# Kernel tuning notes

Measured on AMD Instinct MI355X. Metric: run time of the kernel, lower is better.

## Reference

```python
import jax, jax.numpy as jnp
import numpy as np

B, C, Hh, Ww = 32, 512, 6, 40
NC = 97   # num classes; padding_idx = NC-1, start_idx = NC-2
L = 26    # label length (max_len+1); decoder tokens T = L+1 = 27


def _lstm2(x, layers):
    """2-layer unidirectional LSTM, batch_first, PyTorch gate order (i,f,g,o).
    x: (B,T,D); layers: list of (Wih, Whh, bih, bhh). Returns (B,T,H)."""
    h = x
    for (Wih, Whh, bih, bhh) in layers:
        Hd = Whh.shape[1]
        b = bih + bhh
        def step(carry, xt, Wih=Wih, Whh=Whh, b=b):
            hh, cc = carry
            g = xt @ Wih.T + hh @ Whh.T + b
            i, f, gg, o = jnp.split(g, 4, axis=-1)
            cc = jax.nn.sigmoid(f) * cc + jax.nn.sigmoid(i) * jnp.tanh(gg)
            hh = jax.nn.sigmoid(o) * jnp.tanh(cc)
            return (hh, cc), hh
        init = (jnp.zeros((h.shape[0], Hd), h.dtype), jnp.zeros((h.shape[0], Hd), h.dtype))
        _, ys = jax.lax.scan(step, init, jnp.swapaxes(h, 0, 1))
        h = jnp.swapaxes(ys, 0, 1)
    return h


def setup_inputs() -> dict:
    key = jax.random.key(0)
    it = iter(jax.random.split(key, 48))
    def nrm(shape, s=0.02):
        return jax.random.normal(next(it), shape, jnp.float32) * s
    d = {}
    d['feat'] = jax.random.normal(next(it), (B, C, Hh, Ww), jnp.float32)
    d['label'] = jax.random.randint(next(it), (B, L), 0, NC)
    d['valid_ratios'] = jax.random.uniform(next(it), (B,), jnp.float32, 0.5, 1.0)
    # encoder LSTM (2 layers, 512->512)
    for p in ['e0', 'e1']:
        d[p + '_Wih'] = nrm((4 * C, C)); d[p + '_Whh'] = nrm((4 * C, C))
        d[p + '_bih'] = jnp.zeros((4 * C,), jnp.float32); d[p + '_bhh'] = jnp.zeros((4 * C,), jnp.float32)
    d['enc_W'] = nrm((C, C)); d['enc_b'] = jnp.zeros((C,), jnp.float32)
    # attention: query 1x1 (Linear), key conv3x3, score 1x1 (Linear d->1)
    d['q_W'] = nrm((C, C)); d['q_b'] = jnp.zeros((C,), jnp.float32)
    d['k_W'] = nrm((C, C, 3, 3)); d['k_b'] = jnp.zeros((C,), jnp.float32)
    d['s_W'] = nrm((1, C)); d['s_b'] = jnp.zeros((1,), jnp.float32)
    emb = nrm((NC, C), 1.0)
    d['emb'] = emb.at[NC - 1].set(0.0)  # padding_idx row is zero
    # decoder LSTM (2 layers, 512->512)
    for p in ['d0', 'd1']:
        d[p + '_Wih'] = nrm((4 * C, C)); d[p + '_Whh'] = nrm((4 * C, C))
        d[p + '_bih'] = jnp.zeros((4 * C,), jnp.float32); d[p + '_bhh'] = jnp.zeros((4 * C,), jnp.float32)
    d['pred_W'] = nrm((NC, 3 * C)); d['pred_b'] = jnp.zeros((NC,), jnp.float32)
    return d


def reference(feat, label, valid_ratios,
              e0_Wih, e0_Whh, e0_bih, e0_bhh, e1_Wih, e1_Whh, e1_bih, e1_bhh,
              enc_W, enc_b, q_W, q_b, k_W, k_b, s_W, s_b, emb,
              d0_Wih, d0_Whh, d0_bih, d0_bhh, d1_Wih, d1_Whh, d1_bih, d1_bhh,
              pred_W, pred_b):
    # --- SAREncoder: max-pool over height, 2-layer LSTM, linear on last step ---
    feat_v = jnp.max(feat, axis=2).transpose(0, 2, 1)  # (B, W, C)
    hf = _lstm2(feat_v, [(e0_Wih, e0_Whh, e0_bih, e0_bhh), (e1_Wih, e1_Whh, e1_bih, e1_bhh)])
    holistic = hf[:, -1, :] @ enc_W.T + enc_b  # (B, C)
    # --- tokens: [holistic, embed(label)] ---
    tok = jnp.concatenate([holistic[:, None, :], emb[label]], axis=1)  # (B, T=L+1, C)
    Hid = _lstm2(tok, [(d0_Wih, d0_Whh, d0_bih, d0_bhh), (d1_Wih, d1_Whh, d1_bih, d1_bhh)])
    # --- 2D additive attention ---
    q = Hid @ q_W.T + q_b  # (B, T, C)
    k = jax.lax.conv_general_dilated(feat, k_W, (1, 1), 'SAME',
                                     dimension_numbers=('NCHW', 'OIHW', 'NCHW')) + k_b[None, :, None, None]
    t = jnp.tanh(k[:, None] + q[:, :, :, None, None])  # (B, T, C, h, w) big intermediate
    score = jnp.einsum('btchw,c->bthw', t, s_W[0]) + s_b[0]  # (B, T, h, w)
    vw = jnp.minimum(Ww, jnp.ceil(Ww * valid_ratios)).astype(jnp.int32)  # (B,)
    colmask = jnp.arange(Ww)[None, :] >= vw[:, None]  # (B, w)
    score = jnp.where(colmask[:, None, None, :], -jnp.inf, score)
    T = score.shape[1]
    aw = jax.nn.softmax(score.reshape(score.shape[0], T, -1), axis=-1).reshape(score.shape[0], T, Hh, Ww)
    attn_feat = jnp.einsum('bchw,bthw->btc', feat, aw)  # (B, T, C)
    # --- prediction (pred_concat=True); dropout is identity (deterministic) ---
    hol = jnp.broadcast_to(holistic[:, None, :], Hid.shape)
    preds = jnp.concatenate([Hid, attn_feat, hol], axis=-1) @ pred_W.T + pred_b
    return preds[:, 1:, :]  # (B, L, NC)
```

## Files before the change

### kernel.cpp

```cpp
#include <hip/hip_runtime.h>

typedef unsigned short u16;
typedef __attribute__((ext_vector_type(8))) short short8;
typedef __attribute__((ext_vector_type(4))) float floatx4;
typedef _Float16 half8 __attribute__((ext_vector_type(8)));
typedef _Float16 half2v __attribute__((ext_vector_type(2)));
typedef unsigned uint4v __attribute__((ext_vector_type(4)));

#define AGENT __HIP_MEMORY_SCOPE_AGENT
#define SENT 0x7FFF7FFFu

__device__ __forceinline__ float bf2f(u16 v) { return __uint_as_float(((unsigned)v) << 16); }
__device__ __forceinline__ u16 f2bf(float f) {
    unsigned u = __float_as_uint(f);
    unsigned r = (u + 0x7FFFu + ((u >> 16) & 1u)) >> 16;
    return (u16)r;
}
__device__ __forceinline__ float sigm_(float x) {
    return __builtin_amdgcn_rcpf(1.f + __expf(-x));
}
__device__ __forceinline__ float tanh_(float x) {
    x = fminf(fmaxf(x, -15.f), 15.f);
    float e = __expf(2.f * x);
    return (e - 1.f) * __builtin_amdgcn_rcpf(e + 1.f);
}

typedef __attribute__((address_space(1))) void gvoid_t;
typedef __attribute__((address_space(3))) void lvoid_t;
__device__ __forceinline__ void gl_lds16(const void* g, void* l) {
    __builtin_amdgcn_global_load_lds((gvoid_t*)g, (lvoid_t*)l, 16, 0, 0);
}

#define HEX_WORDS (134 * 32 * 256)

struct SrcPtrs {
    const void* e0Wih; const void* e1Wih; const void* d0Wih; const void* d1Wih;
    const void* b0; const void* b1; const void* b2; const void* b3;
    const void* b4; const void* b5; const void* b6; const void* b7;
    const void* encW; const void* qW; const void* predW; const void* emb;
    const void* encb; const void* qb; const void* kb; const void* sW;
    const void* sb; const void* predb;
};
#define OFF_W0      0
#define OFF_W1      1048576
#define OFF_W2      2097152
#define OFF_W3      3145728
#define OFF_B       4194304
#define OFF_ENCW    4210688
#define OFF_QW      4472832
#define OFF_PREDW   4734976
#define OFF_EMB     4883968
#define OFF_ENCB    4933632
#define OFF_QB      4934144
#define OFF_KB      4934656
#define OFF_SW      4935168
#define OFF_SB      4935680
#define OFF_PREDB   4935681
#define CANON_TOTAL 4935778

__device__ __forceinline__ int sniff_(const void* feat_raw) {
    const u16* p = (const u16*)feat_raw;
    int insane = 0;
    #pragma unroll
    for (int i = 0; i < 32; i += 2) {
        float x = bf2f(p[i]);
        float a = fabsf(x);
        if (!(a <= 1000.f)) insane = 1;
        if (x != 0.f && a < 1e-8f) insane = 1;
    }
    return insane;
}

struct PrepArgs {
    SrcPtrs S;
    const void* feat_raw;
    const void* vr_src;
    const void* kW_src;
    const void* wq_s0; const void* wq_s1; const void* wq_s2; const void* wq_s3;
    int* flag;
    unsigned* hEx;
    u16* canon;
    float* cvr;
    u16* W2;
    _Float16* wq_d0; _Float16* wq_d1; _Float16* wq_d2; _Float16* wq_d3;
    u16* featv;
    u16* featP;
};

#define PB_INIT    0
#define PB_CANON   4288
#define PB_CANONF  23569
#define PB_W2      23570
#define PB_WQ3     32786
#define PB_FEATP   34834
#define PB_TOTAL   35346

__global__ __launch_bounds__(256) void prep_all(PrepArgs P)
{
    const int blk = blockIdx.x;
    const int tid = threadIdx.x;

    if (blk < PB_CANON) {
        int idx = blk * 256 + tid;
        P.hEx[idx] = SENT;
        if (idx == 0) *P.flag = sniff_(P.feat_raw);
        return;
    }
    const int fl = sniff_(P.feat_raw);

    if (blk < PB_CANONF) {
        int idx = (blk - PB_CANON) * 256 + tid;
        if (idx >= CANON_TOTAL) return;
        const SrcPtrs& S = P.S;
        const void* s; int loc;
        if (idx < OFF_B) {
            int k = idx >> 20; loc = idx & 1048575;
            s = (k == 0) ? S.e0Wih : (k == 1) ? S.e1Wih : (k == 2) ? S.d0Wih : S.d1Wih;
        } else if (idx < OFF_ENCW) {
            int r = idx - OFF_B; int k = r >> 11; loc = r & 2047;
            s = (k == 0) ? S.b0 : (k == 1) ? S.b1 : (k == 2) ? S.b2 : (k == 3) ? S.b3
              : (k == 4) ? S.b4 : (k == 5) ? S.b5 : (k == 6) ? S.b6 : S.b7;
        } else if (idx < OFF_QW)    { s = S.encW;  loc = idx - OFF_ENCW; }
        else if (idx < OFF_PREDW)   { s = S.qW;    loc = idx - OFF_QW; }
        else if (idx < OFF_EMB)     { s = S.predW; loc = idx - OFF_PREDW; }
        else if (idx < OFF_ENCB)    { s = S.emb;   loc = idx - OFF_EMB; }
        else if (idx < OFF_QB)      { s = S.encb;  loc = idx - OFF_ENCB; }
        else if (idx < OFF_KB)      { s = S.qb;    loc = idx - OFF_QB; }
        else if (idx < OFF_SW)      { s = S.kb;    loc = idx - OFF_KB; }
        else if (idx < OFF_SB)      { s = S.sW;    loc = idx - OFF_SW; }
        else if (idx < OFF_PREDB)   { s = S.sb;    loc = idx - OFF_SB; }
        else                        { s = S.predb; loc = idx - OFF_PREDB; }
        P.canon[idx] = fl ? f2bf(((const float*)s)[loc]) : ((const u16*)s)[loc];
    } else if (blk == PB_CANONF) {
        if (tid < 32)
            P.cvr[tid] = fl ? ((const float*)P.vr_src)[tid] : bf2f(((const u16*)P.vr_src)[tid]);
    } else if (blk < PB_WQ3) {
        int idx = (blk - PB_W2) * 256 + tid;
        int co = idx / 4608;
        int r = idx % 4608;
        int kh = r / 1536;
        int r2 = r % 1536;
        int kw = r2 / 512;
        int ci = r2 & 511;
        long si = ((long)(co * 512 + ci) * 3 + kh) * 3 + kw;
        P.W2[idx] = fl ? f2bf(((const float*)P.kW_src)[si]) : ((const u16*)P.kW_src)[si];
    } else if (blk < PB_FEATP) {
        int gb = blk - PB_WQ3;
        int id = gb >> 9;
        const void* W = (id == 0) ? P.wq_s0 : (id == 1) ? P.wq_s1 : (id == 2) ? P.wq_s2 : P.wq_s3;
        _Float16* D = (id == 0) ? P.wq_d0 : (id == 1) ? P.wq_d1 : (id == 2) ? P.wq_d2 : P.wq_d3;
        int o = (gb & 511) * 256 + tid;
        int t = o & 511;
        int c = (o >> 9) & 31;
        int j = o >> 14;
        int rid = t >> 1, hf = t & 1;
        int n = (rid >> 6) * 512 + j * 64 + (rid & 63);
        int k = hf * 256 + c * 8;
        _Float16* dst = D + (long)o * 8;
        #pragma unroll
        for (int jj = 0; jj < 8; jj++) {
            long si = (long)n * 512 + k + jj;
            float v = fl ? ((const float*)W)[si] : bf2f(((const u16*)W)[si]);
            dst[jj] = (_Float16)v;
        }
    } else {
        __shared__ u16 S[32][242];
        int q = blk - PB_FEATP;
        int b = q >> 4;
        int c0 = (q & 15) * 32;
        long gbase = ((long)b * 512 + c0) * 240;
        for (int i = tid; i < 32 * 240; i += 256) {
            float x = fl ? ((const float*)P.feat_raw)[gbase + i] : bf2f(((const u16*)P.feat_raw)[gbase + i]);
            S[i / 240][i % 240] = f2bf(x);
        }
        __syncthreads();
        for (int i = tid; i < 40 * 32; i += 256) {
            int w = i >> 5, c = i & 31;
            float mx = bf2f(S[c][w]);
            #pragma unroll
            for (int h = 1; h < 6; h++) mx = fmaxf(mx, bf2f(S[c][h * 40 + w]));
            P.featv[((long)(b * 40 + w)) * 512 + c0 + c] = f2bf(mx);
        }
        for (int i = tid; i < 6 * 40 * 32; i += 256) {
            int c = i & 31; int r = i >> 5;
            int wp1 = r % 40, hp1 = r / 40;
            P.featP[((long)(b * 8 + hp1 + 1) * 42 + (wp1 + 1)) * 512 + c0 + c] = S[c][hp1 * 40 + wp1];
        }
        for (int i = tid; i < 96 * 32; i += 256) {
            int c = i & 31; int r = i >> 5;
            int hp, wp;
            if (r < 42)      { hp = 0; wp = r; }
            else if (r < 84) { hp = 7; wp = r - 42; }
            else             { int q2 = r - 84; hp = 1 + (q2 >> 1); wp = (q2 & 1) * 41; }
            P.featP[((long)(b * 8 + hp) * 42 + wp) * 512 + c0 + c] = 0;
        }
    }
}

__global__ __launch_bounds__(256) void gemm_nt_f32(
    const u16* __restrict__ A, int lda,
    const u16* __restrict__ Bw,
    const u16* __restrict__ bias0, const u16* __restrict__ bias1,
    float* __restrict__ C, int M, int N, int K, int ldc)
{
    __shared__ __align__(16) u16 As[64][40];
    __shared__ __align__(16) u16 Bs[64][40];
    const int tid = threadIdx.x;
    const int bn = blockIdx.x, bm = blockIdx.y;
    const int l = tid & 63, wid = tid >> 6;
    const int wm = wid >> 1, wn = wid & 1;
    const int lr = tid >> 2, lc = (tid & 3) * 8;
    const int l15 = l & 15, lq = l >> 4;

    floatx4 acc00 = (floatx4)(0.f), acc01 = (floatx4)(0.f), acc10 = (floatx4)(0.f), acc11 = (floatx4)(0.f);

    int am = bm * 64 + lr; if (am > M - 1) am = M - 1;
    const u16* Ap = A + (long)am * lda + lc;
    const u16* Bp = Bw + (long)(bn * 64 + lr) * K + lc;

    for (int k0 = 0; k0 < K; k0 += 32) {
        *(short8*)&As[lr][lc] = *(const short8*)(Ap + k0);
        *(short8*)&Bs[lr][lc] = *(const short8*)(Bp + k0);
        __syncthreads();
        short8 af0 = *(const short8*)&As[wm * 32 + l15][lq * 8];
        short8 af1 = *(const short8*)&As[wm * 32 + 16 + l15][lq * 8];
        short8 bf0 = *(const short8*)&Bs[wn * 32 + l15][lq * 8];
        short8 bf1 = *(const short8*)&Bs[wn * 32 + 16 + l15][lq * 8];
        acc00 = __builtin_amdgcn_mfma_f32_16x16x32_bf16(af0, bf0, acc00, 0, 0, 0);
        acc01 = __builtin_amdgcn_mfma_f32_16x16x32_bf16(af0, bf1, acc01, 0, 0, 0);
        acc10 = __builtin_amdgcn_mfma_f32_16x16x32_bf16(af1, bf0, acc10, 0, 0, 0);
        acc11 = __builtin_amdgcn_mfma_f32_16x16x32_bf16(af1, bf1, acc11, 0, 0, 0);
        __syncthreads();
    }
    floatx4 accs[2][2] = {{acc00, acc01}, {acc10, acc11}};
    #pragma unroll
    for (int i = 0; i < 2; i++)
        #pragma unroll
        for (int j = 0; j < 2; j++)
            #pragma unroll
            for (int r = 0; r < 4; r++) {
                int gm = bm * 64 + wm * 32 + i * 16 + lq * 4 + r;
                int gn = bn * 64 + wn * 32 + j * 16 + l15;
                if (gm < M) {
                    float v = accs[i][j][r];
                    if (bias0) v += bf2f(bias0[gn]);
                    if (bias1) v += bf2f(bias1[gn]);
                    C[(long)gm * ldc + gn] = v;
                }
            }
}

__device__ __forceinline__ void gemm128_body(
    u16* lds, const u16* __restrict__ A, const u16* __restrict__ Bw,
    const u16* __restrict__ bias0, const u16* __restrict__ bias1,
    float* __restrict__ C, int M, int ldc, int bn, int bm)
{
    u16 (*As)[128][32] = (u16(*)[128][32])lds;
    u16 (*Bs)[128][32] = (u16(*)[128][32])(lds + 4 * 128 * 32);
    const int tid = threadIdx.x;
    const int wv = tid >> 6, l = tid & 63;
    const int wm = wv >> 2, wn = wv & 3;
    const int l15 = l & 15, lq = l >> 4;
    const int ch = ((l & 3) ^ ((l >> 3) & 3)) * 8;

    int ar = bm * 128 + wv * 16 + (l >> 2);
    if (ar > M - 1) ar = M - 1;
    const u16* ga = A + (long)ar * 512 + ch;
    const u16* gb = Bw + (long)(bn * 128 + wv * 16 + (l >> 2)) * 512 + ch;

    floatx4 acc[4][2];
    #pragma unroll
    for (int i = 0; i < 4; i++)
        #pragma unroll
        for (int j = 0; j < 2; j++) acc[i][j] = (floatx4)(0.f);

    auto stage = [&](int k0, int pb) {
        gl_lds16(ga + k0, &As[pb][wv * 16][0]);
        gl_lds16(gb + k0, &Bs[pb][wv * 16][0]);
    };
    const int rs = (lq ^ ((l15 >> 1) & 3)) * 8;
    auto compute = [&](int cur) {
        short8 af[4], bf[2];
        #pragma unroll
        for (int i = 0; i < 4; i++) af[i] = *(const short8*)&As[cur][wm * 64 + i * 16 + l15][rs];
        #pragma unroll
        for (int j = 0; j < 2; j++) bf[j] = *(const short8*)&Bs[cur][wn * 32 + j * 16 + l15][rs];
        #pragma unroll
        for (int i = 0; i < 4; i++)
            #pragma unroll
            for (int j = 0; j < 2; j++)
                acc[i][j] = __builtin_amdgcn_mfma_f32_16x16x32_bf16(af[i], bf[j], acc[i][j], 0, 0, 0);
    };

    stage(0, 0); stage(32, 1); stage(64, 2);
    for (int k = 0; k < 14; k++) {
        asm volatile("s_waitcnt vmcnt(4)" ::: "memory");
        __builtin_amdgcn_s_barrier();
        asm volatile("" ::: "memory");
        if (k < 13) stage((k + 3) * 32, (k + 3) & 3);
        compute(k & 3);
    }
    asm volatile("s_waitcnt vmcnt(2)" ::: "memory");
    __builtin_amdgcn_s_barrier();
    asm volatile("" ::: "memory");
    compute(2);
    asm volatile("s_waitcnt vmcnt(0)" ::: "memory");
    __builtin_amdgcn_s_barrier();
    asm volatile("" ::: "memory");
    compute(3);

    #pragma unroll
    for (int i = 0; i < 4; i++)
        #pragma unroll
        for (int j = 0; j < 2; j++)
            #pragma unroll
            for (int r = 0; r < 4; r++) {
                int gm = bm * 128 + wm * 64 + i * 16 + lq * 4 + r;
                int gn = bn * 128 + wn * 32 + j * 16 + l15;
                if (gm < M) {
                    float v = acc[i][j][r];
                    if (bias0) v += bf2f(bias0[gn]);
                    if (bias1) v += bf2f(bias1[gn]);
                    C[(long)gm * ldc + gn] = v;
                }
            }
}

__device__ __forceinline__ void conv_body(
    u16* lds, const u16* __restrict__ featP, const u16* __restrict__ W2,
    const u16* __restrict__ kb, u16* __restrict__ kmap, int bx, int by)
{
    u16 (*As)[128][32] = (u16(*)[128][32])lds;
    u16 (*Bs)[128][32] = (u16(*)[128][32])(lds + 4 * 128 * 32);
    const int tid = threadIdx.x;
    int bm = bx * 8 + (by & 7);
    int bn = by >> 3;
    if (bm >= 60) return;
    const int wv = tid >> 6, l = tid & 63;
    const int wm = wv >> 2, wn = wv & 3;
    const int l15 = l & 15, lq = l >> 4;
    const int ch = ((l & 3) ^ ((l >> 3) & 3)) * 8;

    int ar = bm * 128 + wv * 16 + (l >> 2);
    int ab = ar / 240, ahw = ar % 240;
    const u16* ga = featP + ((long)(ab * 8 + ahw / 40) * 42 + (ahw % 40)) * 512 + ch;
    const u16* gb = W2 + (long)(bn * 128 + wv * 16 + (l >> 2)) * 4608 + ch;

    floatx4 acc[4][2];
    #pragma unroll
    for (int i = 0; i < 4; i++)
        #pragma unroll
        for (int j = 0; j < 2; j++) acc[i][j] = (floatx4)(0.f);

    auto stage = [&](int k0, int pb) {
        int kh = k0 / 1536;
        int rem = k0 - kh * 1536;
        int aoff = (kh * 42 + (rem >> 9)) * 512 + (rem & 511);
        gl_lds16(ga + aoff, &As[pb][wv * 16][0]);
        gl_lds16(gb + k0, &Bs[pb][wv * 16][0]);
    };
    const int rs = (lq ^ ((l15 >> 1) & 3)) * 8;
    auto compute = [&](int cur) {
        short8 af[4], bf[2];
        #pragma unroll
        for (int i = 0; i < 4; i++) af[i] = *(const short8*)&As[cur][wm * 64 + i * 16 + l15][rs];
        #pragma unroll
        for (int j = 0; j < 2; j++) bf[j] = *(const short8*)&Bs[cur][wn * 32 + j * 16 + l15][rs];
        #pragma unroll
        for (int i = 0; i < 4; i++)
            #pragma unroll
            for (int j = 0; j < 2; j++)
                acc[i][j] = __builtin_amdgcn_mfma_f32_16x16x32_bf16(af[i], bf[j], acc[i][j], 0, 0, 0);
    };

    stage(0, 0); stage(32, 1); stage(64, 2);
    for (int k = 0; k < 142; k++) {
        asm volatile("s_waitcnt vmcnt(4)" ::: "memory");
        __builtin_amdgcn_s_barrier();
        asm volatile("" ::: "memory");
        if (k < 141) stage((k + 3) * 32, (k + 3) & 3);
        compute(k & 3);
    }
    asm volatile("s_waitcnt vmcnt(2)" ::: "memory");
    __builtin_amdgcn_s_barrier();
    asm volatile("" ::: "memory");
    compute(2);
    asm volatile("s_waitcnt vmcnt(0)" ::: "memory");
    __builtin_amdgcn_s_barrier();
    asm volatile("" ::: "memory");
    compute(3);

    #pragma unroll
    for (int i = 0; i < 4; i++)
        #pragma unroll
        for (int j = 0; j < 2; j++)
            #pragma unroll
            for (int r = 0; r < 4; r++) {
                int row = bm * 128 + wm * 64 + i * 16 + lq * 4 + r;
                int col = bn * 128 + wn * 32 + j * 16 + l15;
                kmap[(long)row * 512 + col] = f2bf(acc[i][j][r] + bf2f(kb[col]));
            }
}

__global__ __launch_bounds__(512) void gemm_nt_128(
    const u16* __restrict__ A, const u16* __restrict__ Bw,
    const u16* __restrict__ bias0, const u16* __restrict__ bias1,
    float* __restrict__ C, int M, int ldc)
{
    extern __shared__ u16 ldsb[];
    gemm128_body(ldsb, A, Bw, bias0, bias1, C, M, ldc, blockIdx.x, blockIdx.y);
}

__global__ __launch_bounds__(512) void qf_conv(
    const u16* __restrict__ Hid, const u16* __restrict__ qW,
    const u16* __restrict__ qb, float* __restrict__ qf,
    const u16* __restrict__ featP, const u16* __restrict__ W2,
    const u16* __restrict__ kb, u16* __restrict__ kmap)
{
    extern __shared__ u16 ldsb[];
    int q = blockIdx.x;
    if (q < 28) {
        gemm128_body(ldsb, Hid, qW, qb, nullptr, qf, 864, 512, q & 3, q >> 2);
    } else {
        int c = q - 28;
        conv_body(ldsb, featP, W2, kb, kmap, c & 7, c >> 3);
    }
}

#define WL(F) F(0) F(1) F(2) F(3) F(4) F(5) F(6) F(7) F(8) F(9) F(10) F(11) F(12) F(13) F(14) F(15) \
              F(16) F(17) F(18) F(19) F(20) F(21) F(22) F(23) F(24) F(25) F(26) F(27) F(28) F(29) F(30) F(31)
#define WLA(F) F(0,0) F(1,1) F(2,2) F(3,3) F(4,0) F(5,1) F(6,2) F(7,3) \
               F(8,0) F(9,1) F(10,2) F(11,3) F(12,0) F(13,1) F(14,2) F(15,3) \
               F(16,0) F(17,1) F(18,2) F(19,3) F(20,0) F(21,1) F(22,2) F(23,3) \
               F(24,0) F(25,1) F(26,2) F(27,3) F(28,0) F(29,1) F(30,2) F(31,3)
#define WDECL(i) half8 w##i = wp8[(long)(j * 32 + i) * 512 + tid];
#define WPIN(i)  asm volatile("" : "+v"(w##i));
#define DOTC(i,k) { \
    half8 hv = *(const half8*)&hS2[(hf * 2 + (i / 16)) * 136 + (i % 16) * 8]; \
    a##k = __builtin_amdgcn_fdot2(__builtin_shufflevector(hv, hv, 0, 1), __builtin_shufflevector(w##i, w##i, 0, 1), a##k, false); \
    a##k = __builtin_amdgcn_fdot2(__builtin_shufflevector(hv, hv, 2, 3), __builtin_shufflevector(w##i, w##i, 2, 3), a##k, false); \
    a##k = __builtin_amdgcn_fdot2(__builtin_shufflevector(hv, hv, 4, 5), __builtin_shufflevector(w##i, w##i, 4, 5), a##k, false); \
    a##k = __builtin_amdgcn_fdot2(__builtin_shufflevector(hv, hv, 6, 7), __builtin_shufflevector(w##i, w##i, 6, 7), a##k, false); }

__global__ __launch_bounds__(512) __attribute__((amdgpu_waves_per_eu(2, 2))) void lstm_sync(
    const float* __restrict__ xpre, const _Float16* __restrict__ Wq3,
    u16* __restrict__ seq_out, float* __restrict__ f32_out,
    unsigned* __restrict__ hExT, int T, int f32_ld)
{
    const int i_ = blockIdx.x;
    const int slot = i_ >> 3;
    const int b = (i_ & 7) * 4 + (slot & 3);
    const int j = slot >> 2;
    const int tid = threadIdx.x;
    const int hf = tid & 1;

    __shared__ __align__(16) _Float16 hS2[4 * 136];
    __shared__ float part[512];

    const half8* wp8 = (const half8*)Wq3;
    WL(WDECL)
    WL(WPIN)
    float cst = 0.f;

    for (int t = 0; t < T; t++) {
        float xi = 0.f, xf = 0.f, xg = 0.f, xo = 0.f;
        if (tid < 64) {
            const float* xp = xpre + ((long)b * T + t) * 2048 + j * 64 + tid;
            xi = xp[0]; xf = xp[512]; xg = xp[1024]; xo = xp[1536];
        }
        float a0 = 0.f, a1 = 0.f, a2 = 0.f, a3 = 0.f;
        if (t > 0) {
            if (tid < 64) {
                const unsigned* src = &hExT[((long)(t - 1) * 32 + b) * 256 + tid * 4];
                unsigned v0, v1, v2, v3;
                do {
                    v0 = __hip_atomic_load(src + 0, __ATOMIC_RELAXED, AGENT);
                    v1 = __hip_atomic_load(src + 1, __ATOMIC_RELAXED, AGENT);
                    v2 = __hip_atomic_load(src + 2, __ATOMIC_RELAXED, AGENT);
                    v3 = __hip_atomic_load(src + 3, __ATOMIC_RELAXED, AGENT);
                } while (v0 == SENT || v1 == SENT || v2 == SENT || v3 == SENT);
                uint4v v; v.x = v0; v.y = v1; v.z = v2; v.w = v3;
                *(uint4v*)&hS2[(tid >> 4) * 136 + (tid & 15) * 8] = v;
            }
            __syncthreads();
            WLA(DOTC)
        }
        part[tid] = (a0 + a1) + (a2 + a3);
        __syncthreads();
        if (tid < 64) {
            float gi = xi + part[(0   + tid) * 2] + part[(0   + tid) * 2 + 1];
            float gf = xf + part[(64  + tid) * 2] + part[(64  + tid) * 2 + 1];
            float gg = xg + part[(128 + tid) * 2] + part[(128 + tid) * 2 + 1];
            float go = xo + part[(192 + tid) * 2] + part[(192 + tid) * 2 + 1];
            cst = sigm_(gf) * cst + sigm_(gi) * tanh_(gg);
            float h = sigm_(go) * tanh_(cst);
            float hlo = __shfl(h, tid * 2);
            float hhi = __shfl(h, tid * 2 + 1);
            if (t + 1 < T && tid < 32) {
                half2v hp; hp[0] = (_Float16)hlo; hp[1] = (_Float16)hhi;
                __hip_atomic_store(&hExT[((long)t * 32 + b) * 256 + j * 32 + tid],
                                   *(unsigned*)&hp, __ATOMIC_RELAXED, AGENT);
            }
            asm volatile("" ::: "memory");
            long so = ((long)b * T + t) * 512 + j * 64 + tid;
            seq_out[so] = f2bf(h);
            if (f32_out) f32_out[((long)b * T + t) * f32_ld + j * 64 + tid] = h;
        }
    }
}

__global__ __launch_bounds__(256) void tok_k(
    const float* __restrict__ holf, const u16* __restrict__ cemb,
    const int* __restrict__ label, u16* __restrict__ tok)
{
    int idx = blockIdx.x * 256 + threadIdx.x;
    int c = idx & 511;
    int m = idx >> 9;
    int b = m / 27, t = m % 27;
    float v;
    if (t == 0) v = holf[(long)b * 512 + c];
    else v = bf2f(cemb[(long)label[b * 26 + (t - 1)] * 512 + c]);
    tok[idx] = f2bf(v);
}

__global__ __launch_bounds__(256) void score_k(
    const float* __restrict__ q, const u16* __restrict__ kmap,
    const u16* __restrict__ sW, const u16* __restrict__ sb,
    const float* __restrict__ vr, float* __restrict__ aw)
{
    int blk = blockIdx.x;
    int xcd = blk & 7, rest = blk >> 3;
    int bq = rest & 3, t = rest >> 2;
    int b = xcd * 4 + bq;
    int bt = b * 27 + t;
    int tid = threadIdx.x, wv = tid >> 6, ln = tid & 63;

    __shared__ float sc[240];
    __shared__ float red[256];

    float qr[8], sr[8];
    const float* qp = q + (long)bt * 512 + ln * 8;
    #pragma unroll
    for (int i = 0; i < 8; i++) qr[i] = qp[i];
    #pragma unroll
    for (int i = 0; i < 8; i++) sr[i] = bf2f(sW[ln * 8 + i]);

    const u16* kb_ = kmap + (long)b * 240 * 512;
    for (int r = wv * 60; r < wv * 60 + 60; r++) {
        short8 kv = *(const short8*)(kb_ + (long)r * 512 + ln * 8);
        float acc = 0.f;
        #pragma unroll
        for (int i = 0; i < 8; i++) {
            float x = bf2f((u16)kv[i]) + qr[i];
            acc = fmaf(sr[i], tanh_(x), acc);
        }
        #pragma unroll
        for (int m = 32; m > 0; m >>= 1) acc += __shfl_xor(acc, m);
        if (ln == 0) sc[r] = acc;
    }
    __syncthreads();

    float scv = -INFINITY, ex = 0.f;
    if (tid < 240) {
        float rr = vr[b];
        int vw = (int)ceilf(40.f * rr);
        if (vw > 40) vw = 40;
        int wcol = tid % 40;
        scv = (wcol >= vw) ? -INFINITY : (sc[tid] + bf2f(sb[0]));
    }
    red[tid] = scv;
    __syncthreads();
    for (int s = 128; s > 0; s >>= 1) {
        if (tid < s) red[tid] = fmaxf(red[tid], red[tid + s]);
        __syncthreads();
    }
    float mx = red[0];
    __syncthreads();
    if (tid < 240) ex = (scv == -INFINITY) ? 0.f : __expf(scv - mx);
    red[tid] = ex;
    __syncthreads();
    for (int s = 128; s > 0; s >>= 1) {
        if (tid < s) red[tid] += red[tid + s];
        __syncthreads();
    }
    float inv = __builtin_amdgcn_rcpf(red[0]);
    if (tid < 240) aw[(long)bt * 240 + tid] = ex * inv;
}

__global__ __launch_bounds__(256) void attn_k(
    const void* __restrict__ feat, const float* __restrict__ aw,
    float* __restrict__ concat, const int* __restrict__ flag)
{
    const int fl = *flag;
    int b = blockIdx.x >> 3;
    int cc = (blockIdx.x & 7) * 64;
    int tid = threadIdx.x;
    __shared__ float awS[27 * 240];
    __shared__ u16 fS[64 * 240];
    for (int i = tid; i < 27 * 240; i += 256) awS[i] = aw[(long)b * 27 * 240 + i];
    long fbase = ((long)b * 512 + cc) * 240;
    for (int i = tid; i < 64 * 240; i += 256)
        fS[i] = fl ? f2bf(((const float*)feat)[fbase + i]) : ((const u16*)feat)[fbase + i];
    __syncthreads();
    for (int item = tid; item < 64 * 27; item += 256) {
        int c = item / 27, t = item % 27;
        const u16* fp = &fS[c * 240];
        const float* ap = &awS[t * 240];
        float acc = 0.f;
        for (int hw = 0; hw < 240; hw++) acc = fmaf(bf2f(fp[hw]), ap[hw], acc);
        concat[((long)(b * 27 + t)) * 1536 + 512 + cc + c] = acc;
    }
}

__global__ __launch_bounds__(256) void pred_k(
    const float* __restrict__ concat, const float* __restrict__ holf,
    const u16* __restrict__ pW, const u16* __restrict__ pb,
    void* __restrict__ out, const int* __restrict__ flag)
{
    int m0 = blockIdx.x * 4;
    int tid = threadIdx.x;
    const int fl = *flag;
    __shared__ float aS[4][1024];
    __shared__ float hS[4][512];
    for (int i = tid; i < 4 * 1024; i += 256)
        aS[i / 1024][i % 1024] = concat[(long)(m0 + i / 1024) * 1536 + (i % 1024)];
    for (int i = tid; i < 4 * 512; i += 256) {
        int m = m0 + i / 512;
        hS[i / 512][i % 512] = holf[(long)(m / 27) * 512 + (i % 512)];
    }
    __syncthreads();
    int r = tid >> 6;
    int nb = tid & 63;
    int m = m0 + r;
    int b = m / 27, t = m % 27;
    for (int n = nb; n < 97; n += 64) {
        const u16* wp = pW + (long)n * 1536;
        float acc = 0.f;
        for (int k0 = 0; k0 < 1024; k0 += 8) {
            short8 wv8 = *(const short8*)(wp + k0);
            #pragma unroll
            for (int q = 0; q < 8; q++) acc = fmaf(aS[r][k0 + q], bf2f((u16)wv8[q]), acc);
        }
        for (int k0 = 0; k0 < 512; k0 += 8) {
            short8 wv8 = *(const short8*)(wp + 1024 + k0);
            #pragma unroll
            for (int q = 0; q < 8; q++) acc = fmaf(hS[r][k0 + q], bf2f((u16)wv8[q]), acc);
        }
        acc += bf2f(pb[n]);
        if (t > 0) {
            long o = ((long)(b * 26 + (t - 1))) * 97 + n;
            if (fl) ((float*)out)[o] = acc;
            else    ((u16*)out)[o] = f2bf(acc);
        }
    }
}

extern "C" void kernel_launch(void* const* d_in, const int* in_sizes, int n_in,
                              void* d_out, int out_size, void* d_ws, size_t ws_size,
                              hipStream_t stream) {
    (void)in_sizes; (void)n_in; (void)out_size; (void)ws_size;
    const void* feat_r = d_in[0];
    const int*  label  = (const int*)d_in[1];
    const void* vr_r   = d_in[2];

    char* w = (char*)d_ws;
    size_t off = 0;
    auto alloc = [&](size_t bytes) -> void* {
        void* p = w + off;
        off = (off + bytes + 63) & ~(size_t)63;
        return p;
    };
    int*   flag    = (int*)  alloc(4);
    unsigned* hEx  = (unsigned*)alloc((size_t)HEX_WORDS * 4);
    u16*   canon   = (u16*)  alloc((size_t)CANON_TOTAL * 2);
    float* cvr     = (float*)alloc(32ull * 4);
    u16*   featv   = (u16*)  alloc(655360ull * 2);
    float* xpre    = (float*)alloc(2621440ull * 4);
    u16*   seq0    = (u16*)  alloc(655360ull * 2);
    u16*   seq1    = (u16*)  alloc(655360ull * 2);
    u16*   tok     = (u16*)  alloc(442368ull * 2);
    u16*   seqd0   = (u16*)  alloc(442368ull * 2);
    u16*   Hid     = (u16*)  alloc(442368ull * 2);
    float* holf    = (float*)alloc(16384ull * 4);
    float* qf      = (float*)alloc(442368ull * 4);
    u16*   featP   = (u16*)  alloc(5505024ull * 2);
    u16*   W2      = (u16*)  alloc(2359296ull * 2);
    float* aw      = (float*)alloc(207360ull * 4);
    float* concat  = (float*)alloc(1327104ull * 4);
    _Float16* Wq[4];
    for (int i = 0; i < 4; i++) Wq[i] = (_Float16*)alloc(1048576ull * 2);
    u16*   kmap    = (u16*)xpre;

    unsigned* hEx0 = hEx;
    unsigned* hEx1 = hEx + 40ull * 8192;
    unsigned* hEx2 = hEx + 80ull * 8192;
    unsigned* hEx3 = hEx + 107ull * 8192;

    u16* cW0    = canon + OFF_W0;
    u16* cW1    = canon + OFF_W1;
    u16* cW2    = canon + OFF_W2;
    u16* cW3    = canon + OFF_W3;
    u16* cb0    = canon + OFF_B;
    u16* cencW  = canon + OFF_ENCW;
    u16* cqW    = canon + OFF_QW;
    u16* cpredW = canon + OFF_PREDW;
    u16* cemb   = canon + OFF_EMB;
    u16* cencb  = canon + OFF_ENCB;
    u16* cqb    = canon + OFF_QB;
    u16* ckb    = canon + OFF_KB;
    u16* csW    = canon + OFF_SW;
    u16* csb    = canon + OFF_SB;
    u16* cpredb = canon + OFF_PREDB;

    PrepArgs P;
    P.S.e0Wih = d_in[3];  P.S.e1Wih = d_in[7];  P.S.d0Wih = d_in[20]; P.S.d1Wih = d_in[24];
    P.S.b0 = d_in[5];  P.S.b1 = d_in[6];  P.S.b2 = d_in[9];  P.S.b3 = d_in[10];
    P.S.b4 = d_in[22]; P.S.b5 = d_in[23]; P.S.b6 = d_in[26]; P.S.b7 = d_in[27];
    P.S.encW = d_in[11]; P.S.qW = d_in[13]; P.S.predW = d_in[28]; P.S.emb = d_in[19];
    P.S.encb = d_in[12]; P.S.qb = d_in[14]; P.S.kb = d_in[16]; P.S.sW = d_in[17];
    P.S.sb = d_in[18]; P.S.predb = d_in[29];
    P.feat_raw = feat_r; P.vr_src = vr_r; P.kW_src = d_in[15];
    P.wq_s0 = d_in[4]; P.wq_s1 = d_in[8]; P.wq_s2 = d_in[21]; P.wq_s3 = d_in[25];
    P.flag = flag; P.hEx = hEx; P.canon = canon; P.cvr = cvr;
    P.W2 = W2;
    P.wq_d0 = Wq[0]; P.wq_d1 = Wq[1]; P.wq_d2 = Wq[2]; P.wq_d3 = Wq[3];
    P.featv = featv; P.featP = featP;
    prep_all<<<dim3(PB_TOTAL), 256, 0, stream>>>(P);

    gemm_nt_128<<<dim3(16, 10), 512, 65536, stream>>>(featv, cW0, cb0 + 0 * 2048, cb0 + 1 * 2048, xpre, 1280, 2048);
    lstm_sync<<<dim3(256), 512, 0, stream>>>(xpre, Wq[0], seq0, nullptr, hEx0, 40, 0);
    gemm_nt_128<<<dim3(16, 10), 512, 65536, stream>>>(seq0, cW1, cb0 + 2 * 2048, cb0 + 3 * 2048, xpre, 1280, 2048);
    lstm_sync<<<dim3(256), 512, 0, stream>>>(xpre, Wq[1], seq1, nullptr, hEx1, 40, 0);
    gemm_nt_f32<<<dim3(8, 1), 256, 0, stream>>>(seq1 + 39 * 512, 40 * 512, cencW, cencb, nullptr, holf, 32, 512, 512, 512);

    tok_k<<<dim3(1728), 256, 0, stream>>>(holf, cemb, label, tok);
    gemm_nt_128<<<dim3(16, 7), 512, 65536, stream>>>(tok, cW2, cb0 + 4 * 2048, cb0 + 5 * 2048, xpre, 864, 2048);
    lstm_sync<<<dim3(256), 512, 0, stream>>>(xpre, Wq[2], seqd0, nullptr, hEx2, 27, 0);
    gemm_nt_128<<<dim3(16, 7), 512, 65536, stream>>>(seqd0, cW3, cb0 + 6 * 2048, cb0 + 7 * 2048, xpre, 864, 2048);
    lstm_sync<<<dim3(256), 512, 0, stream>>>(xpre, Wq[3], Hid, concat, hEx3, 27, 1536);

    qf_conv<<<dim3(284), 512, 65536, stream>>>(Hid, cqW, cqb, qf, featP, W2, ckb, kmap);
    score_k<<<dim3(864), 256, 0, stream>>>(qf, kmap, csW, csb, cvr, aw);
    attn_k<<<dim3(256), 256, 0, stream>>>(feat_r, aw, concat, flag);

    pred_k<<<dim3(216), 256, 0, stream>>>(concat, holf, cpredW, cpredb, d_out, flag);
}
```

Measured before the change: 733.0 us.

## Skip weight canonicalization when inputs already bf16; fuse encoder projection with token build

The prep kernel now skips copying the large Wih weights, encoder, and query matrices into the canonical buffer when the sniffed input format flag is clear. The GEMM kernels then read the raw input pointers directly, chosen at runtime from the flag. The encoder-output projection and token assembly are fused into one kernel, which writes the holistic row into tok directly and copies the embedding rows without an f32 round trip. This removes a large prep copy and one launch, at the cost of a flag load in every GEMM block.

After: 724.7 us. About the same (-1.1%).

```diff
diff --git a/kernel.cpp b/kernel.cpp
--- a/kernel.cpp
+++ b/kernel.cpp
@@ -111,6 +111,7 @@
     if (blk < PB_CANONF) {
         int idx = (blk - PB_CANON) * 256 + tid;
         if (idx >= CANON_TOTAL) return;
+        if (!fl && idx < OFF_PREDW) return;
         const SrcPtrs& S = P.S;
         const void* s; int loc;
         if (idx < OFF_B) {
@@ -197,64 +198,13 @@
     }
 }
 
-__global__ __launch_bounds__(256) void gemm_nt_f32(
-    const u16* __restrict__ A, int lda,
-    const u16* __restrict__ Bw,
-    const u16* __restrict__ bias0, const u16* __restrict__ bias1,
-    float* __restrict__ C, int M, int N, int K, int ldc)
-{
-    __shared__ __align__(16) u16 As[64][40];
-    __shared__ __align__(16) u16 Bs[64][40];
-    const int tid = threadIdx.x;
-    const int bn = blockIdx.x, bm = blockIdx.y;
-    const int l = tid & 63, wid = tid >> 6;
-    const int wm = wid >> 1, wn = wid & 1;
-    const int lr = tid >> 2, lc = (tid & 3) * 8;
-    const int l15 = l & 15, lq = l >> 4;
-
-    floatx4 acc00 = (floatx4)(0.f), acc01 = (floatx4)(0.f), acc10 = (floatx4)(0.f), acc11 = (floatx4)(0.f);
-
-    int am = bm * 64 + lr; if (am > M - 1) am = M - 1;
-    const u16* Ap = A + (long)am * lda + lc;
-    const u16* Bp = Bw + (long)(bn * 64 + lr) * K + lc;
-
-    for (int k0 = 0; k0 < K; k0 += 32) {
-        *(short8*)&As[lr][lc] = *(const short8*)(Ap + k0);
-        *(short8*)&Bs[lr][lc] = *(const short8*)(Bp + k0);
-        __syncthreads();
-        short8 af0 = *(const short8*)&As[wm * 32 + l15][lq * 8];
-        short8 af1 = *(const short8*)&As[wm * 32 + 16 + l15][lq * 8];
-        short8 bf0 = *(const short8*)&Bs[wn * 32 + l15][lq * 8];
-        short8 bf1 = *(const short8*)&Bs[wn * 32 + 16 + l15][lq * 8];
-        acc00 = __builtin_amdgcn_mfma_f32_16x16x32_bf16(af0, bf0, acc00, 0, 0, 0);
-        acc01 = __builtin_amdgcn_mfma_f32_16x16x32_bf16(af0, bf1, acc01, 0, 0, 0);
-        acc10 = __builtin_amdgcn_mfma_f32_16x16x32_bf16(af1, bf0, acc10, 0, 0, 0);
-        acc11 = __builtin_amdgcn_mfma_f32_16x16x32_bf16(af1, bf1, acc11, 0, 0, 0);
-        __syncthreads();
-    }
-    floatx4 accs[2][2] = {{acc00, acc01}, {acc10, acc11}};
-    #pragma unroll
-    for (int i = 0; i < 2; i++)
-        #pragma unroll
-        for (int j = 0; j < 2; j++)
-            #pragma unroll
-            for (int r = 0; r < 4; r++) {
-                int gm = bm * 64 + wm * 32 + i * 16 + lq * 4 + r;
-                int gn = bn * 64 + wn * 32 + j * 16 + l15;
-                if (gm < M) {
-                    float v = accs[i][j][r];
-                    if (bias0) v += bf2f(bias0[gn]);
-                    if (bias1) v += bf2f(bias1[gn]);
-                    C[(long)gm * ldc + gn] = v;
-                }
-            }
-}
-
 __device__ __forceinline__ void gemm128_body(
-    u16* lds, const u16* __restrict__ A, const u16* __restrict__ Bw,
+    u16* lds, const u16* __restrict__ A,
+    const u16* __restrict__ Bcanon, const u16* __restrict__ Braw, const int* __restrict__ flag,
     const u16* __restrict__ bias0, const u16* __restrict__ bias1,
     float* __restrict__ C, int M, int ldc, int bn, int bm)
 {
+    const u16* Bw = (*flag) ? Bcanon : Braw;
     u16 (*As)[128][32] = (u16(*)[128][32])lds;
     u16 (*Bs)[128][32] = (u16(*)[128][32])(lds + 4 * 128 * 32);
     const int tid = threadIdx.x;
@@ -403,27 +353,91 @@
 }
 
 __global__ __launch_bounds__(512) void gemm_nt_128(
-    const u16* __restrict__ A, const u16* __restrict__ Bw,
+    const u16* __restrict__ A,
+    const u16* __restrict__ Bcanon, const u16* __restrict__ Braw,
     const u16* __restrict__ bias0, const u16* __restrict__ bias1,
-    float* __restrict__ C, int M, int ldc)
+    float* __restrict__ C, int M, int ldc, const int* __restrict__ flag)
 {
     extern __shared__ u16 ldsb[];
-    gemm128_body(ldsb, A, Bw, bias0, bias1, C, M, ldc, blockIdx.x, blockIdx.y);
+    gemm128_body(ldsb, A, Bcanon, Braw, flag, bias0, bias1, C, M, ldc, blockIdx.x, blockIdx.y);
 }
 
 __global__ __launch_bounds__(512) void qf_conv(
-    const u16* __restrict__ Hid, const u16* __restrict__ qW,
+    const u16* __restrict__ Hid, const u16* __restrict__ qWc, const u16* __restrict__ qWr,
     const u16* __restrict__ qb, float* __restrict__ qf,
     const u16* __restrict__ featP, const u16* __restrict__ W2,
-    const u16* __restrict__ kb, u16* __restrict__ kmap)
+    const u16* __restrict__ kb, u16* __restrict__ kmap, const int* __restrict__ flag)
 {
     extern __shared__ u16 ldsb[];
     int q = blockIdx.x;
     if (q < 28) {
-        gemm128_body(ldsb, Hid, qW, qb, nullptr, qf, 864, 512, q & 3, q >> 2);
+        gemm128_body(ldsb, Hid, qWc, qWr, flag, qb, nullptr, qf, 864, 512, q & 3, q >> 2);
     } else {
         int c = q - 28;
         conv_body(ldsb, featP, W2, kb, kmap, c & 7, c >> 3);
+    }
+}
+
+__global__ __launch_bounds__(256) void enc_tok(
+    const u16* __restrict__ A, int lda,
+    const u16* __restrict__ Bcanon, const u16* __restrict__ Braw,
+    const u16* __restrict__ bias0,
+    float* __restrict__ holf, u16* __restrict__ tok,
+    const u16* __restrict__ cemb, const int* __restrict__ label,
+    const int* __restrict__ flag)
+{
+    if (blockIdx.x < 8) {
+        const u16* Bw = (*flag) ? Bcanon : Braw;
+        __shared__ __align__(16) u16 As[64][40];
+        __shared__ __align__(16) u16 Bs[64][40];
+        const int tid = threadIdx.x;
+        const int bn = blockIdx.x;
+        const int l = tid & 63, wid = tid >> 6;
+        const int wm = wid >> 1, wn = wid & 1;
+        const int lr = tid >> 2, lc = (tid & 3) * 8;
+        const int l15 = l & 15, lq = l >> 4;
+
+        floatx4 acc00 = (floatx4)(0.f), acc01 = (floatx4)(0.f), acc10 = (floatx4)(0.f), acc11 = (floatx4)(0.f);
+
+        int am = lr; if (am > 31) am = 31;
+        const u16* Ap = A + (long)am * lda + lc;
+        const u16* Bp = Bw + (long)(bn * 64 + lr) * 512 + lc;
+
+        for (int k0 = 0; k0 < 512; k0 += 32) {
+            *(short8*)&As[lr][lc] = *(const short8*)(Ap + k0);
+            *(short8*)&Bs[lr][lc] = *(const short8*)(Bp + k0);
+            __syncthreads();
+            short8 af0 = *(const short8*)&As[wm * 32 + l15][lq * 8];
+            short8 af1 = *(const short8*)&As[wm * 32 + 16 + l15][lq * 8];
+            short8 bf0 = *(const short8*)&Bs[wn * 32 + l15][lq * 8];
+            short8 bf1 = *(const short8*)&Bs[wn * 32 + 16 + l15][lq * 8];
+            acc00 = __builtin_amdgcn_mfma_f32_16x16x32_bf16(af0, bf0, acc00, 0, 0, 0);
+            acc01 = __builtin_amdgcn_mfma_f32_16x16x32_bf16(af0, bf1, acc01, 0, 0, 0);
+            acc10 = __builtin_amdgcn_mfma_f32_16x16x32_bf16(af1, bf0, acc10, 0, 0, 0);
+            acc11 = __builtin_amdgcn_mfma_f32_16x16x32_bf16(af1, bf1, acc11, 0, 0, 0);
+            __syncthreads();
+        }
+        floatx4 accs[2][2] = {{acc00, acc01}, {acc10, acc11}};
+        #pragma unroll
+        for (int i = 0; i < 2; i++)
+            #pragma unroll
+            for (int j = 0; j < 2; j++)
+                #pragma unroll
+                for (int r = 0; r < 4; r++) {
+                    int gm = wm * 32 + i * 16 + lq * 4 + r;
+                    int gn = bn * 64 + wn * 32 + j * 16 + l15;
+                    if (gm < 32) {
+                        float v = accs[i][j][r] + bf2f(bias0[gn]);
+                        holf[(long)gm * 512 + gn] = v;
+                        tok[(long)gm * 27 * 512 + gn] = f2bf(v);
+                    }
+                }
+    } else {
+        int idx = (blockIdx.x - 8) * 256 + threadIdx.x;
+        int c = idx & 511;
+        int m2 = idx >> 9;
+        int b = m2 / 26, t = m2 % 26 + 1;
+        tok[((long)(b * 27 + t)) * 512 + c] = cemb[(long)label[b * 26 + (t - 1)] * 512 + c];
     }
 }
 
@@ -507,20 +521,6 @@
             if (f32_out) f32_out[((long)b * T + t) * f32_ld + j * 64 + tid] = h;
         }
     }
-}
-
-__global__ __launch_bounds__(256) void tok_k(
-    const float* __restrict__ holf, const u16* __restrict__ cemb,
-    const int* __restrict__ label, u16* __restrict__ tok)
-{
-    int idx = blockIdx.x * 256 + threadIdx.x;
-    int c = idx & 511;
-    int m = idx >> 9;
-    int b = m / 27, t = m % 27;
-    float v;
-    if (t == 0) v = holf[(long)b * 512 + c];
-    else v = bf2f(cemb[(long)label[b * 26 + (t - 1)] * 512 + c]);
-    tok[idx] = f2bf(v);
 }
 
 __global__ __launch_bounds__(256) void score_k(
@@ -727,19 +727,19 @@
     P.featv = featv; P.featP = featP;
     prep_all<<<dim3(PB_TOTAL), 256, 0, stream>>>(P);
 
-    gemm_nt_128<<<dim3(16, 10), 512, 65536, stream>>>(featv, cW0, cb0 + 0 * 2048, cb0 + 1 * 2048, xpre, 1280, 2048);
+    gemm_nt_128<<<dim3(16, 10), 512, 65536, stream>>>(featv, cW0, (const u16*)d_in[3], cb0 + 0 * 2048, cb0 + 1 * 2048, xpre, 1280, 2048, flag);
     lstm_sync<<<dim3(256), 512, 0, stream>>>(xpre, Wq[0], seq0, nullptr, hEx0, 40, 0);
-    gemm_nt_128<<<dim3(16, 10), 512, 65536, stream>>>(seq0, cW1, cb0 + 2 * 2048, cb0 + 3 * 2048, xpre, 1280, 2048);
+    gemm_nt_128<<<dim3(16, 10), 512, 65536, stream>>>(seq0, cW1, (const u16*)d_in[7], cb0 + 2 * 2048, cb0 + 3 * 2048, xpre, 1280, 2048, flag);
     lstm_sync<<<dim3(256), 512, 0, stream>>>(xpre, Wq[1], seq1, nullptr, hEx1, 40, 0);
-    gemm_nt_f32<<<dim3(8, 1), 256, 0, stream>>>(seq1 + 39 * 512, 40 * 512, cencW, cencb, nullptr, holf, 32, 512, 512, 512);
-
-    tok_k<<<dim3(1728), 256, 0, stream>>>(holf, cemb, label, tok);
-    gemm_nt_128<<<dim3(16, 7), 512, 65536, stream>>>(tok, cW2, cb0 + 4 * 2048, cb0 + 5 * 2048, xpre, 864, 2048);
+
+    enc_tok<<<dim3(1672), 256, 0, stream>>>(seq1 + 39 * 512, 40 * 512, cencW, (const u16*)d_in[11],
+                                            cencb, holf, tok, cemb, label, flag);
+    gemm_nt_128<<<dim3(16, 7), 512, 65536, stream>>>(tok, cW2, (const u16*)d_in[20], cb0 + 4 * 2048, cb0 + 5 * 2048, xpre, 864, 2048, flag);
     lstm_sync<<<dim3(256), 512, 0, stream>>>(xpre, Wq[2], seqd0, nullptr, hEx2, 27, 0);
-    gemm_nt_128<<<dim3(16, 7), 512, 65536, stream>>>(seqd0, cW3, cb0 + 6 * 2048, cb0 + 7 * 2048, xpre, 864, 2048);
+    gemm_nt_128<<<dim3(16, 7), 512, 65536, stream>>>(seqd0, cW3, (const u16*)d_in[24], cb0 + 6 * 2048, cb0 + 7 * 2048, xpre, 864, 2048, flag);
     lstm_sync<<<dim3(256), 512, 0, stream>>>(xpre, Wq[3], Hid, concat, hEx3, 27, 1536);
 
-    qf_conv<<<dim3(284), 512, 65536, stream>>>(Hid, cqW, cqb, qf, featP, W2, ckb, kmap);
+    qf_conv<<<dim3(284), 512, 65536, stream>>>(Hid, cqW, (const u16*)d_in[13], cqb, qf, featP, W2, ckb, kmap, flag);
     score_k<<<dim3(864), 256, 0, stream>>>(qf, kmap, csW, csb, cvr, aw);
     attn_k<<<dim3(256), 256, 0, stream>>>(feat_r, aw, concat, flag);
 
```
